# Kernel tuning notes

Hardware: AMD Instinct MI355X
Metric: run time of the kernel (lower is better)

The kernel has to match this reference:

```python
import jax, jax.numpy as jnp
import numpy as np
import math

BS, NAG, HID, NACT, MESS, QD, KD, STEPS, INP = 4096, 8, 256, 16, 64, 64, 64, 5, 128
TRAJ = STEPS * NACT
LAMQ = 0.5


def setup_inputs() -> dict:
    key = jax.random.key(0)
    ks = jax.random.split(key, 12)
    g = lambda k, shape, fan: jax.random.normal(k, shape, jnp.float32) / math.sqrt(fan)
    d = {}
    d["inputs"] = jax.random.normal(ks[0], (BS * NAG, INP), jnp.float32)
    d["old_hstate"] = jax.random.normal(ks[1], (BS * NAG, HID), jnp.float32)
    d["fc1_w"] = g(ks[2], (HID, INP), INP); d["fc1_b"] = jnp.zeros((HID,), jnp.float32)
    d["w_ih"] = g(ks[3], (3 * HID, HID), HID); d["w_hh"] = g(ks[4], (3 * HID, HID), HID)
    d["b_ih"] = jnp.zeros((3 * HID,), jnp.float32); d["b_hh"] = jnp.zeros((3 * HID,), jnp.float32)
    d["dec_w"] = g(ks[5], (NACT, HID), HID); d["dec_b"] = jnp.zeros((NACT,), jnp.float32)
    d["trans_w"] = g(ks[6], (HID, HID + NAG), HID + NAG); d["trans_b"] = jnp.zeros((HID,), jnp.float32)
    d["qij_w"] = g(ks[7], (NACT, HID + MESS), HID + MESS); d["qij_b"] = jnp.zeros((NACT,), jnp.float32)
    d["q_w"] = g(ks[8], (QD, TRAJ), TRAJ); d["q_b"] = jnp.zeros((QD,), jnp.float32)
    d["k_w"] = g(ks[9], (KD, TRAJ), TRAJ); d["k_b"] = jnp.zeros((KD,), jnp.float32)
    d["v_w"] = g(ks[10], (MESS, TRAJ), TRAJ); d["v_b"] = jnp.zeros((MESS,), jnp.float32)
    return d


def _fwd(inputs, old_hstate, fc1_w, fc1_b, w_ih, w_hh, b_ih, b_hh,
         dec_w, dec_b, trans_w, trans_b, qij_w, qij_b,
         q_w, q_b, k_w, k_b, v_w, v_b):
    # fc1 + relu
    x = jax.nn.relu(inputs @ fc1_w.T + fc1_b)  # (BS*NAG, HID)
    # GRUCell (torch gate order: r, z, n)
    gi = x @ w_ih.T + b_ih
    gh = old_hstate @ w_hh.T + b_hh
    ir, iz, i_n = jnp.split(gi, 3, axis=-1)
    hr, hz, h_n = jnp.split(gh, 3, axis=-1)
    r = jax.nn.sigmoid(ir + hr)
    z = jax.nn.sigmoid(iz + hz)
    n = jnp.tanh(i_n + r * h_n)
    h_new = (1.0 - z) * n + z * old_hstate
    h = h_new.reshape(BS, NAG, HID)

    # imagination rollout on detached h
    def step(hc, _):
        q_inf = hc @ dec_w.T + dec_b                       # (BS, NAG, NACT)
        ac = jnp.argmax(q_inf, axis=-1).astype(hc.dtype)   # (BS, NAG)
        ac = jnp.broadcast_to(ac[:, None, :], (BS, NAG, NAG))
        ti = jnp.concatenate([hc, ac], axis=-1)            # (BS, NAG, HID+NAG)
        return ti @ trans_w.T + trans_b, q_inf

    _, qs = jax.lax.scan(step, jax.lax.stop_gradient(h), None, length=STEPS)
    # qs: (STEPS, BS, NAG, NACT) -> trajectory (BS, NAG, STEPS*NACT), step-major on last dim
    traj = jnp.moveaxis(qs, 0, 2).reshape(BS, NAG, TRAJ)

    # tiny agent attention
    query = traj @ q_w.T + q_b   # (BS, NAG, QD)
    key_t = traj @ k_w.T + k_b   # (BS, NAG, KD)
    value = traj @ v_w.T + v_b   # (BS, NAG, MESS)
    score = jnp.einsum('bnq,bmq->bnm', query, key_t) / math.sqrt(MESS)
    attn = jax.nn.softmax(score, axis=-1)
    traj_msg = jnp.einsum('bnm,bmd->bnd', attn, value)  # (BS, NAG, MESS)

    q_local = h @ dec_w.T + dec_b
    q_ij = jnp.concatenate([h, traj_msg], axis=-1) @ qij_w.T + qij_b
    q = q_local + LAMQ * q_ij
    return q, h


def reference(inputs, old_hstate, fc1_w, fc1_b, w_ih, w_hh, b_ih, b_hh,
              dec_w, dec_b, trans_w, trans_b, qij_w, qij_b,
              q_w, q_b, k_w, k_b, v_w, v_b):
    return _fwd(inputs, old_hstate, fc1_w, fc1_b, w_ih, w_hh, b_ih, b_hh,
                dec_w, dec_b, trans_w, trans_b, qij_w, qij_b,
                q_w, q_b, k_w, k_b, v_w, v_b)
```

## Files before the change

kernel.cpp:

```cpp
#include <hip/hip_runtime.h>
#include <math.h>

typedef unsigned short u16;
typedef unsigned int   u32;
typedef __attribute__((ext_vector_type(8))) short bf16x8;
typedef __attribute__((ext_vector_type(4))) float f32x4;

#define NROWS 32768
#define NAG 8
#define HID 256
#define INP 128
#define NACT 16
#define MESS 64
#define TRAJD 80
#define QD 64
#define HOFF 524288

#define PKO_FC1 0
#define PKO_IH  98304
#define PKO_HH  688128
#define PKO_TR  1277952
#define PKO_DEC 1499136
#define PKO_QKV 1511424
#define PKO_QIJ 1566720
#define PK_TOTAL 1582080
#define WS_CB   791040
#define WS_FLAG 793312

#define OB_FC1B 0
#define OB_BIH  256
#define OB_BHH  1024
#define OB_DECB 1792
#define OB_TRB  1808
#define OB_QIJB 2064
#define OB_QB   2080

__device__ __forceinline__ float bf2f(u16 v){ return __uint_as_float(((u32)v)<<16); }
__device__ __forceinline__ u16 f2bf(float f){
    u32 u = __float_as_uint(f);
    return (u16)((u + 0x7fffu + ((u>>16)&1u))>>16);
}
__device__ __forceinline__ float sig_(float x){ return 1.0f/(1.0f+expf(-x)); }
__device__ __forceinline__ float ldin(const void* p, size_t i, int f32){
    return f32 ? ((const float*)p)[i] : bf2f(((const u16*)p)[i]);
}
__device__ __forceinline__ void stout1(void* out, size_t i, float v, int f32){
    if (f32) ((float*)out)[i]=v; else ((u16*)out)[i]=f2bf(v);
}
__device__ __forceinline__ void split3(float w, u16& s0, u16& s1, u16& s2){
    u16 a=f2bf(w); float r  = w - bf2f(a);
    u16 b=f2bf(r); float r2 = r - bf2f(b);
    s0=a; s1=b; s2=f2bf(r2);
}
__device__ __forceinline__ f32x4 splat4(float b){ f32x4 v = {b,b,b,b}; return v; }

#define MFMA(a,b,c) __builtin_amdgcn_mfma_f32_16x16x32_bf16((a),(b),(c),0,0,0)

__device__ __forceinline__ bf16x8 lda_pl(const u16* P, int p, int row, int kbyte){
    const char* b = (const char*)P + ((p*32+row)*640) + (kbyte ^ ((row&7)<<4));
    return *(const bf16x8*)b;
}
__device__ __forceinline__ void stw_pl(u16* P, int p, int row, int col, u16 v){
    char* b = (char*)P + ((p*32+row)*640) + (((col*2)) ^ ((row&7)<<4));
    *(u16*)b = v;
}
__device__ __forceinline__ void split_store_pl(u16* P, int row, int col, float v){
    u16 a,b,c; split3(v,a,b,c);
    stw_pl(P,0,row,col,a); stw_pl(P,1,row,col,b); stw_pl(P,2,row,col,c);
}
__device__ __forceinline__ bf16x8 lda_tp(const u16* P, int p, int row, int kbyte){
    const char* b = (const char*)P + ((p*32+row)*256) + (kbyte ^ ((row&7)<<4));
    return *(const bf16x8*)b;
}
__device__ __forceinline__ void stw_tp(u16* P, int p, int row, int col, u16 v){
    char* b = (char*)P + ((p*32+row)*256) + (((col*2)) ^ ((row&7)<<4));
    *(u16*)b = v;
}
__device__ __forceinline__ void split_store_tp(u16* P, int row, int col, float v){
    u16 a,b,c; split3(v,a,b,c);
    stw_tp(P,0,row,col,a); stw_tp(P,1,row,col,b); stw_tp(P,2,row,col,c);
}
__device__ __forceinline__ float ld_tp1(const u16* P, int p, int row, int col){
    const char* b = (const char*)P + ((p*32+row)*256) + (((col*2)) ^ ((row&7)<<4));
    return bf2f(*(const u16*)b);
}
__device__ __forceinline__ bf16x8 ldg_bf8(const void* p, size_t off){
    return *(const bf16x8*)((const u16*)p + off);
}
__device__ __forceinline__ void ldg_f32_split(const void* p, size_t off, bf16x8& f0, bf16x8& f1, bf16x8& f2){
    const float* fp = (const float*)p + off;
    #pragma unroll
    for (int j=0;j<8;j++){
        float w = fp[j];
        u16 a,b,c; split3(w,a,b,c);
        f0[j]=(short)a; f1[j]=(short)b; f2[j]=(short)c;
    }
}
#define BCH(base, NTv, ksv, pbv, ntv) \
    (*(const bf16x8*)((base) + ((((ksv)*3+(pbv))*(NTv) + (ntv))*512) + lane*8))

__global__ void k_det(const void* __restrict__ inp, int* __restrict__ flag){
    __shared__ int cnt;
    if (threadIdx.x==0) cnt=0;
    __syncthreads();
    int big=0;
    for (int i=threadIdx.x;i<128;i+=64){
        u32 w = ((const u32*)inp)[i];
        float g = bf2f((u16)w);
        if (!(fabsf(g) <= 1e4f)) big++;
    }
    if (big) atomicAdd(&cnt, big);
    __syncthreads();
    if (threadIdx.x==0) *flag = (cnt>=4) ? 1 : 0;
}

__device__ __forceinline__ void pack_tile(const void* W, int Kdim, int NT, u16* pk, int tau, int f32){
    int lane2 = tau & 63, c = tau >> 6;
    int nt = c % NT, ks = c / NT;
    int n  = nt*16 + (lane2 & 15);
    int kb = ks*32 + (lane2 >> 4)*8;
    u16 o0[8],o1[8],o2[8];
    #pragma unroll
    for (int j=0;j<8;j++){
        int k = kb + j;
        float w = (k < Kdim) ? ldin(W, (size_t)n*Kdim + k, f32) : 0.0f;
        split3(w, o0[j], o1[j], o2[j]);
    }
    size_t base = ((size_t)(ks*3+0)*NT + nt)*512 + lane2*8;
    size_t step = (size_t)NT*512;
    #pragma unroll
    for (int j=0;j<8;j++){
        pk[base+j]=o0[j]; pk[base+step+j]=o1[j]; pk[base+2*step+j]=o2[j];
    }
}

__global__ __launch_bounds__(256) void k0_prep(
    const void* fc1_w, const void* w_ih, const void* w_hh, const void* trans_w,
    const void* dec_w, const void* qij_w, const void* q_w, const void* k_w, const void* v_w,
    const void* fc1_b, const void* b_ih, const void* b_hh, const void* dec_b,
    const void* trans_b, const void* qij_b, const void* q_b, const void* k_b, const void* v_b,
    float* __restrict__ ws, const int* __restrict__ flagp)
{
    const int f32 = *flagp;
    u16* pk = (u16*)ws;
    int i = blockIdx.x*256 + threadIdx.x;
    if (i < 4096)        pack_tile(fc1_w,  128, 16, pk+PKO_FC1, i,        f32);
    else if (i < 28672)  pack_tile(w_ih,   256, 48, pk+PKO_IH,  i-4096,   f32);
    else if (i < 53248)  pack_tile(w_hh,   256, 48, pk+PKO_HH,  i-28672,  f32);
    else if (i < 62464)  pack_tile(trans_w,264, 16, pk+PKO_TR,  i-53248,  f32);
    else if (i < 62976)  pack_tile(dec_w,  256,  1, pk+PKO_DEC, i-62464,  f32);
    else if (i < 65280){
        int tau = i - 62976;
        int lane2 = tau&63, c = tau>>6, nt = c%12, ks = c/12;
        int n = nt*16 + (lane2&15);
        const void* W = (n<64)? q_w : (n<128 ? k_w : v_w);
        int nl = n & 63;
        int kb = ks*32 + (lane2>>4)*8;
        u16 o0[8],o1[8],o2[8];
        #pragma unroll
        for (int j=0;j<8;j++){
            int k = kb + j;
            float w = (k < 80) ? ldin(W, (size_t)nl*80 + k, f32) : 0.0f;
            split3(w, o0[j], o1[j], o2[j]);
        }
        u16* dst = pk + PKO_QKV;
        size_t base = ((size_t)(ks*3+0)*12 + nt)*512 + lane2*8;
        size_t step = (size_t)12*512;
        #pragma unroll
        for (int j=0;j<8;j++){
            dst[base+j]=o0[j]; dst[base+step+j]=o1[j]; dst[base+2*step+j]=o2[j];
        }
    }
    else if (i < 65920)  pack_tile(qij_w,  320,  1, pk+PKO_QIJ, i-65280,  f32);
    else if (i < 68192){
        int i2 = i - 65920;
        float v;
        if      (i2<256)  v=ldin(fc1_b,i2,f32);
        else if (i2<1024) v=ldin(b_ih,i2-256,f32);
        else if (i2<1792) v=ldin(b_hh,i2-1024,f32);
        else if (i2<1808) v=ldin(dec_b,i2-1792,f32);
        else if (i2<2064) v=ldin(trans_b,i2-1808,f32);
        else if (i2<2080) v=ldin(qij_b,i2-2064,f32);
        else if (i2<2144) v=ldin(q_b,i2-2080,f32);
        else if (i2<2208) v=ldin(k_b,i2-2144,f32);
        else              v=ldin(v_b,i2-2208,f32);
        ws[WS_CB+i2]=v;
    }
}

template<int F32>
__global__ __launch_bounds__(512,2) void k12_fused(
    const void* __restrict__ inp, const void* __restrict__ oldh,
    const float* __restrict__ ws, void* __restrict__ dout, const int* __restrict__ flagp)
{
    if (*flagp != F32) return;
    constexpr int PBW = F32 ? 2 : 0;
    constexpr int PAG = F32 ? 2 : 0;

    __shared__ __align__(16) u16  planes[3*32*320];
    __shared__ __align__(16) u16  tplanes[3*32*128];
    __shared__ float s_qkv[32*201];
    __shared__ float s_att[256];
    __shared__ float s_bias[2272];
    __shared__ float s_act[32];

    const int t = threadIdx.x;
    const int wid = t>>6, lane = t&63, lr = lane&15, lk = lane>>4;
    const int row0 = blockIdx.x*32;
    const u16* pk = (const u16*)ws;
    const float* cb = ws + WS_CB;

    for (int i=t;i<3*32*320/2;i+=512) ((u32*)planes)[i]=0u;
    for (int i=t;i<3*32*128/2;i+=512) ((u32*)tplanes)[i]=0u;
    for (int i=t;i<2272;i+=512) s_bias[i]=cb[i];
    __syncthreads();

    {
        const u16* pkf = pk + PKO_FC1;
        const int nt0 = wid, nt1 = wid + 8;
        f32x4 acc[2][2];
        acc[0][0]=splat4(s_bias[OB_FC1B+nt0*16+lr]); acc[1][0]=acc[0][0];
        acc[0][1]=splat4(s_bias[OB_FC1B+nt1*16+lr]); acc[1][1]=acc[0][1];
        for (int ks=0;ks<4;ks++){
            bf16x8 a[2][3];
            if (F32){
                ldg_f32_split(inp,(size_t)(row0+lr)*INP + ks*32+lk*8,    a[0][0],a[0][1],a[0][2]);
                ldg_f32_split(inp,(size_t)(row0+16+lr)*INP + ks*32+lk*8, a[1][0],a[1][1],a[1][2]);
            } else {
                a[0][0]=ldg_bf8(inp,(size_t)(row0+lr)*INP + ks*32+lk*8);
                a[1][0]=ldg_bf8(inp,(size_t)(row0+16+lr)*INP + ks*32+lk*8);
            }
            #pragma unroll
            for (int pb=0;pb<=PBW;pb++){
                bf16x8 B0 = BCH(pkf,16,ks,pb,nt0);
                bf16x8 B1 = BCH(pkf,16,ks,pb,nt1);
                #pragma unroll
                for (int pa=0;pa<=((PAG<2-pb)?PAG:(2-pb));pa++){
                    acc[0][0]=MFMA(a[0][pa],B0,acc[0][0]); acc[0][1]=MFMA(a[0][pa],B1,acc[0][1]);
                    acc[1][0]=MFMA(a[1][pa],B0,acc[1][0]); acc[1][1]=MFMA(a[1][pa],B1,acc[1][1]);
                }
            }
        }
        #pragma unroll
        for (int m=0;m<2;m++)
        #pragma unroll
        for (int ni=0;ni<2;ni++)
        #pragma unroll
        for (int j=0;j<4;j++){
            float v = acc[m][ni][j]; v = v>0.f ? v : 0.f;
            split_store_pl(planes, m*16+lk*4+j, (ni?nt1:nt0)*16+lr, v);
        }
    }
    __syncthreads();

    float hreg[16];
    {
        const u16* pki = pk + PKO_IH;
        const u16* pkh = pk + PKO_HH;
        const int g0 = wid, g1 = wid + 8;
        f32x4 aR[2][2], aZ[2][2], aN[2][2], aH[2][2];
        #pragma unroll
        for (int m=0;m<2;m++)
        #pragma unroll
        for (int gi=0;gi<2;gi++){
            int c = (gi?g1:g0)*16 + lr;
            aR[m][gi]=splat4(s_bias[OB_BIH+c]     + s_bias[OB_BHH+c]);
            aZ[m][gi]=splat4(s_bias[OB_BIH+256+c] + s_bias[OB_BHH+256+c]);
            aN[m][gi]=splat4(s_bias[OB_BIH+512+c]);
            aH[m][gi]=splat4(s_bias[OB_BHH+512+c]);
        }
        for (int ks=0;ks<8;ks++){
            #pragma unroll
            for (int pb=0;pb<=PBW;pb++){
                bf16x8 Br0=BCH(pki,48,ks,pb,g0),    Br1=BCH(pki,48,ks,pb,g1);
                bf16x8 Bz0=BCH(pki,48,ks,pb,16+g0), Bz1=BCH(pki,48,ks,pb,16+g1);
                bf16x8 Bn0=BCH(pki,48,ks,pb,32+g0), Bn1=BCH(pki,48,ks,pb,32+g1);
                #pragma unroll
                for (int pa=0;pa<=2-pb;pa++){
                    bf16x8 a0 = lda_pl(planes, pa, lr,    ks*64+lk*16);
                    bf16x8 a1 = lda_pl(planes, pa, 16+lr, ks*64+lk*16);
                    aR[0][0]=MFMA(a0,Br0,aR[0][0]); aR[0][1]=MFMA(a0,Br1,aR[0][1]);
                    aR[1][0]=MFMA(a1,Br0,aR[1][0]); aR[1][1]=MFMA(a1,Br1,aR[1][1]);
                    aZ[0][0]=MFMA(a0,Bz0,aZ[0][0]); aZ[0][1]=MFMA(a0,Bz1,aZ[0][1]);
                    aZ[1][0]=MFMA(a1,Bz0,aZ[1][0]); aZ[1][1]=MFMA(a1,Bz1,aZ[1][1]);
                    aN[0][0]=MFMA(a0,Bn0,aN[0][0]); aN[0][1]=MFMA(a0,Bn1,aN[0][1]);
                    aN[1][0]=MFMA(a1,Bn0,aN[1][0]); aN[1][1]=MFMA(a1,Bn1,aN[1][1]);
                }
            }
        }
        for (int ks=0;ks<8;ks++){
            bf16x8 a[2][3];
            if (F32){
                ldg_f32_split(oldh,(size_t)(row0+lr)*HID + ks*32+lk*8,    a[0][0],a[0][1],a[0][2]);
                ldg_f32_split(oldh,(size_t)(row0+16+lr)*HID + ks*32+lk*8, a[1][0],a[1][1],a[1][2]);
            } else {
                a[0][0]=ldg_bf8(oldh,(size_t)(row0+lr)*HID + ks*32+lk*8);
                a[1][0]=ldg_bf8(oldh,(size_t)(row0+16+lr)*HID + ks*32+lk*8);
            }
            #pragma unroll
            for (int pb=0;pb<=PBW;pb++){
                bf16x8 Br0=BCH(pkh,48,ks,pb,g0),    Br1=BCH(pkh,48,ks,pb,g1);
                bf16x8 Bz0=BCH(pkh,48,ks,pb,16+g0), Bz1=BCH(pkh,48,ks,pb,16+g1);
                bf16x8 Bh0=BCH(pkh,48,ks,pb,32+g0), Bh1=BCH(pkh,48,ks,pb,32+g1);
                #pragma unroll
                for (int pa=0;pa<=((PAG<2-pb)?PAG:(2-pb));pa++){
                    aR[0][0]=MFMA(a[0][pa],Br0,aR[0][0]); aR[0][1]=MFMA(a[0][pa],Br1,aR[0][1]);
                    aR[1][0]=MFMA(a[1][pa],Br0,aR[1][0]); aR[1][1]=MFMA(a[1][pa],Br1,aR[1][1]);
                    aZ[0][0]=MFMA(a[0][pa],Bz0,aZ[0][0]); aZ[0][1]=MFMA(a[0][pa],Bz1,aZ[0][1]);
                    aZ[1][0]=MFMA(a[1][pa],Bz0,aZ[1][0]); aZ[1][1]=MFMA(a[1][pa],Bz1,aZ[1][1]);
                    aH[0][0]=MFMA(a[0][pa],Bh0,aH[0][0]); aH[0][1]=MFMA(a[0][pa],Bh1,aH[0][1]);
                    aH[1][0]=MFMA(a[1][pa],Bh0,aH[1][0]); aH[1][1]=MFMA(a[1][pa],Bh1,aH[1][1]);
                }
            }
        }
        #pragma unroll
        for (int m=0;m<2;m++)
        #pragma unroll
        for (int gi=0;gi<2;gi++)
        #pragma unroll
        for (int j=0;j<4;j++){
            int row = m*16 + lk*4 + j;
            int c   = (gi?g1:g0)*16 + lr;
            float r  = sig_(aR[m][gi][j]);
            float z  = sig_(aZ[m][gi][j]);
            float nv = tanhf(aN[m][gi][j] + r*aH[m][gi][j]);
            float ho = ldin(oldh,(size_t)(row0+row)*HID + c, F32);
            float h  = (1.f-z)*nv + z*ho;
            hreg[m*8+gi*4+j] = h;
            stout1(dout,(size_t)HOFF + (size_t)(row0+row)*HID + c, h, F32);
        }
    }
    __syncthreads();
    #pragma unroll
    for (int m=0;m<2;m++)
    #pragma unroll
    for (int gi=0;gi<2;gi++)
    #pragma unroll
    for (int j=0;j<4;j++)
        split_store_pl(planes, m*16+lk*4+j, (gi?wid+8:wid)*16+lr, hreg[m*8+gi*4+j]);
    __syncthreads();

    const u16* pkd = pk + PKO_DEC;
    const u16* pkt = pk + PKO_TR;
    #pragma unroll 1
    for (int s=0;s<5;s++){
        if (wid<2){
            const int m = wid;
            f32x4 d0 = splat4(s_bias[OB_DECB+lr]);
            f32x4 d1 = splat4(0.f), d2 = splat4(0.f);
            for (int ks=0;ks<8;ks++){
                #pragma unroll
                for (int pb=0;pb<=PBW;pb++){
                    bf16x8 B = BCH(pkd,1,ks,pb,0);
                    #pragma unroll
                    for (int pa=0;pa<=2-pb;pa++){
                        bf16x8 a = lda_pl(planes, pa, m*16+lr, ks*64+lk*16);
                        if (pa==0) d0=MFMA(a,B,d0); else if (pa==1) d1=MFMA(a,B,d1); else d2=MFMA(a,B,d2);
                    }
                }
            }
            f32x4 q;
            #pragma unroll
            for (int j=0;j<4;j++) q[j]=d0[j]+d1[j]+d2[j];
            #pragma unroll
            for (int j=0;j<4;j++)
                split_store_tp(tplanes, m*16+lk*4+j, s*16+lr, q[j]);
            if (s<4){
                #pragma unroll
                for (int j=0;j<4;j++){
                    float v = q[j]; int ai = lr;
                    #pragma unroll
                    for (int msk=1; msk<16; msk<<=1){
                        float pv = __shfl_xor(v, msk);
                        int   pi = __shfl_xor(ai, msk);
                        if (pv>v || (pv==v && pi<ai)){ v=pv; ai=pi; }
                    }
                    if (lr==0) s_act[m*16+lk*4+j] = (float)ai;
                }
            }
        }
        if (s==4) break;
        __syncthreads();
        if (t<256){
            int row = t>>3, aj = t&7;
            stw_pl(planes, 0, row, 256+aj, f2bf(s_act[(row & ~7) + aj]));
        }
        __syncthreads();
        {
            const int nt0=wid, nt1=wid+8;
            f32x4 acc[2][2];
            acc[0][0]=splat4(s_bias[OB_TRB+nt0*16+lr]); acc[1][0]=acc[0][0];
            acc[0][1]=splat4(s_bias[OB_TRB+nt1*16+lr]); acc[1][1]=acc[0][1];
            for (int ks=0;ks<9;ks++){
                #pragma unroll
                for (int pb=0;pb<=PBW;pb++){
                    bf16x8 B0=BCH(pkt,16,ks,pb,nt0), B1=BCH(pkt,16,ks,pb,nt1);
                    #pragma unroll
                    for (int pa=0;pa<=2-pb;pa++){
                        bf16x8 a0 = lda_pl(planes,pa,lr,   ks*64+lk*16);
                        bf16x8 a1 = lda_pl(planes,pa,16+lr,ks*64+lk*16);
                        acc[0][0]=MFMA(a0,B0,acc[0][0]); acc[0][1]=MFMA(a0,B1,acc[0][1]);
                        acc[1][0]=MFMA(a1,B0,acc[1][0]); acc[1][1]=MFMA(a1,B1,acc[1][1]);
                    }
                }
            }
            __syncthreads();
            #pragma unroll
            for (int m=0;m<2;m++)
            #pragma unroll
            for (int ni=0;ni<2;ni++)
            #pragma unroll
            for (int j=0;j<4;j++)
                split_store_pl(planes, m*16+lk*4+j, (ni?nt1:nt0)*16+lr, acc[m][ni][j]);
        }
        __syncthreads();
    }

    __syncthreads();
    #pragma unroll
    for (int m=0;m<2;m++)
    #pragma unroll
    for (int gi=0;gi<2;gi++)
    #pragma unroll
    for (int j=0;j<4;j++)
        split_store_pl(planes, m*16+lk*4+j, (gi?wid+8:wid)*16+lr, hreg[m*8+gi*4+j]);
    {
        const u16* pkq = pk + PKO_QKV;
        const int n0 = wid;
        const int has2 = (wid<4);
        const int n1 = wid + 8;
        f32x4 acc[2][2];
        acc[0][0]=splat4(s_bias[OB_QB+n0*16+lr]); acc[1][0]=acc[0][0];
        { float b1 = has2 ? s_bias[OB_QB+n1*16+lr] : 0.f;
          acc[0][1]=splat4(b1); acc[1][1]=acc[0][1]; }
        for (int ks=0;ks<3;ks++){
            #pragma unroll
            for (int pb=0;pb<=PBW;pb++){
                bf16x8 B0 = BCH(pkq,12,ks,pb,n0);
                bf16x8 B1 = has2 ? BCH(pkq,12,ks,pb,n1) : B0;
                #pragma unroll
                for (int pa=0;pa<=2-pb;pa++){
                    bf16x8 a0 = lda_tp(tplanes, pa, lr,    ks*64+lk*16);
                    bf16x8 a1 = lda_tp(tplanes, pa, 16+lr, ks*64+lk*16);
                    acc[0][0]=MFMA(a0,B0,acc[0][0]); acc[1][0]=MFMA(a1,B0,acc[1][0]);
                    if (has2){ acc[0][1]=MFMA(a0,B1,acc[0][1]); acc[1][1]=MFMA(a1,B1,acc[1][1]); }
                }
            }
        }
        #pragma unroll
        for (int m=0;m<2;m++)
        #pragma unroll
        for (int j=0;j<4;j++){
            int row = m*16+lk*4+j;
            s_qkv[row*201 + n0*16+lr] = acc[m][0][j];
            if (has2) s_qkv[row*201 + n1*16+lr] = acc[m][1][j];
        }
    }
    __syncthreads();
    if (t<256){
        int b=t>>6, n=(t>>3)&7, mm=t&7;
        const float* qv = s_qkv + (b*8+n)*201;
        const float* kv = s_qkv + (b*8+mm)*201 + 64;
        float a2=0.f;
        #pragma unroll
        for (int d=0;d<64;d++) a2 += qv[d]*kv[d];
        s_att[t] = a2*0.125f;
    }
    __syncthreads();
    if (t<32){
        int base = (t>>3)*64 + (t&7)*8;
        float mx = s_att[base];
        #pragma unroll
        for (int j2=1;j2<8;j2++) mx = fmaxf(mx, s_att[base+j2]);
        float e[8]; float sum=0.f;
        #pragma unroll
        for (int j2=0;j2<8;j2++){ e[j2]=expf(s_att[base+j2]-mx); sum+=e[j2]; }
        float inv = 1.f/sum;
        #pragma unroll
        for (int j2=0;j2<8;j2++) s_att[base+j2] = e[j2]*inv;
    }
    __syncthreads();
    for (int o=t;o<2048;o+=512){
        int row=o>>6, d=o&63, b=row>>3;
        float a3=0.f;
        #pragma unroll
        for (int mm=0;mm<8;mm++) a3 += s_att[b*64+(row&7)*8+mm]*s_qkv[(b*8+mm)*201+128+d];
        split_store_pl(planes, row, 256+d, a3);
    }
    __syncthreads();
    if (wid<2){
        const u16* pkj = pk + PKO_QIJ;
        const int m = wid;
        f32x4 e0 = splat4(s_bias[OB_QIJB+lr]);
        f32x4 e1 = splat4(0.f), e2 = splat4(0.f);
        for (int ks=0;ks<10;ks++){
            #pragma unroll
            for (int pb=0;pb<=PBW;pb++){
                bf16x8 B = BCH(pkj,1,ks,pb,0);
                #pragma unroll
                for (int pa=0;pa<=2-pb;pa++){
                    bf16x8 a = lda_pl(planes, pa, m*16+lr, ks*64+lk*16);
                    if (pa==0) e0=MFMA(a,B,e0); else if (pa==1) e1=MFMA(a,B,e1); else e2=MFMA(a,B,e2);
                }
            }
        }
        #pragma unroll
        for (int j=0;j<4;j++){
            int row = m*16+lk*4+j;
            float ql = ld_tp1(tplanes,0,row,lr) + ld_tp1(tplanes,1,row,lr) + ld_tp1(tplanes,2,row,lr);
            float qq = ql + 0.5f*(e0[j]+e1[j]+e2[j]);
            stout1(dout,(size_t)(row0+row)*NACT + lr, qq, F32);
        }
    }
}

extern "C" void kernel_launch(void* const* d_in, const int* in_sizes, int n_in,
                              void* d_out, int out_size, void* d_ws, size_t ws_size,
                              hipStream_t stream)
{
    (void)in_sizes; (void)n_in; (void)out_size; (void)ws_size;
    const void* inputs = d_in[0];
    const void* oldh   = d_in[1];
    float* ws = (float*)d_ws;
    int* flagp = (int*)(ws + WS_FLAG);

    k_det<<<1,64,0,stream>>>(inputs, flagp);
    k0_prep<<<268,256,0,stream>>>(d_in[2],d_in[4],d_in[5],d_in[10],d_in[8],d_in[12],
                                  d_in[14],d_in[16],d_in[18],
                                  d_in[3],d_in[6],d_in[7],d_in[9],d_in[11],d_in[13],
                                  d_in[15],d_in[17],d_in[19],
                                  ws, flagp);
    k12_fused<0><<<1024,512,0,stream>>>(inputs, oldh, ws, d_out, flagp);
    k12_fused<1><<<1024,512,0,stream>>>(inputs, oldh, ws, d_out, flagp);
}
```

Measured before the change: 616.8 us.

## Halve rows per block to 16, use 256-thread blocks, keep trajectory in fp32 LDS

Each block now handles 16 rows (two batch groups) with 4 waves, each wave owning 4 output tiles, and the grid doubles to 2048 blocks. The goal is more resident blocks per CU through lower LDS use. The bias staging in LDS is dropped in favour of direct reads from global memory. The trajectory is stored as fp32 in LDS and split into three bf16 parts when the QKV projection loads it. The decoder step and argmax now run redundantly in every wave, so no separate action sync is needed. The trade-off is less reuse of each B-fragment load, since each one now feeds half as many rows, which means more weight traffic from L2.

```diff
diff --git a/kernel.cpp b/kernel.cpp
--- a/kernel.cpp
+++ b/kernel.cpp
@@ -57,32 +57,16 @@
 #define MFMA(a,b,c) __builtin_amdgcn_mfma_f32_16x16x32_bf16((a),(b),(c),0,0,0)
 
 __device__ __forceinline__ bf16x8 lda_pl(const u16* P, int p, int row, int kbyte){
-    const char* b = (const char*)P + ((p*32+row)*640) + (kbyte ^ ((row&7)<<4));
+    const char* b = (const char*)P + ((p*16+row)*640) + (kbyte ^ ((row&7)<<4));
     return *(const bf16x8*)b;
 }
 __device__ __forceinline__ void stw_pl(u16* P, int p, int row, int col, u16 v){
-    char* b = (char*)P + ((p*32+row)*640) + (((col*2)) ^ ((row&7)<<4));
+    char* b = (char*)P + ((p*16+row)*640) + (((col*2)) ^ ((row&7)<<4));
     *(u16*)b = v;
 }
 __device__ __forceinline__ void split_store_pl(u16* P, int row, int col, float v){
     u16 a,b,c; split3(v,a,b,c);
     stw_pl(P,0,row,col,a); stw_pl(P,1,row,col,b); stw_pl(P,2,row,col,c);
-}
-__device__ __forceinline__ bf16x8 lda_tp(const u16* P, int p, int row, int kbyte){
-    const char* b = (const char*)P + ((p*32+row)*256) + (kbyte ^ ((row&7)<<4));
-    return *(const bf16x8*)b;
-}
-__device__ __forceinline__ void stw_tp(u16* P, int p, int row, int col, u16 v){
-    char* b = (char*)P + ((p*32+row)*256) + (((col*2)) ^ ((row&7)<<4));
-    *(u16*)b = v;
-}
-__device__ __forceinline__ void split_store_tp(u16* P, int row, int col, float v){
-    u16 a,b,c; split3(v,a,b,c);
-    stw_tp(P,0,row,col,a); stw_tp(P,1,row,col,b); stw_tp(P,2,row,col,c);
-}
-__device__ __forceinline__ float ld_tp1(const u16* P, int p, int row, int col){
-    const char* b = (const char*)P + ((p*32+row)*256) + (((col*2)) ^ ((row&7)<<4));
-    return bf2f(*(const u16*)b);
 }
 __device__ __forceinline__ bf16x8 ldg_bf8(const void* p, size_t off){
     return *(const bf16x8*)((const u16*)p + off);
@@ -189,7 +173,7 @@
 }
 
 template<int F32>
-__global__ __launch_bounds__(512,2) void k12_fused(
+__global__ __launch_bounds__(256,3) void k12_fused(
     const void* __restrict__ inp, const void* __restrict__ oldh,
     const float* __restrict__ ws, void* __restrict__ dout, const int* __restrict__ flagp)
 {
@@ -197,58 +181,47 @@
     constexpr int PBW = F32 ? 2 : 0;
     constexpr int PAG = F32 ? 2 : 0;
 
-    __shared__ __align__(16) u16  planes[3*32*320];
-    __shared__ __align__(16) u16  tplanes[3*32*128];
-    __shared__ float s_qkv[32*201];
-    __shared__ float s_att[256];
-    __shared__ float s_bias[2272];
-    __shared__ float s_act[32];
+    __shared__ __align__(16) u16   planes[3*16*320];
+    __shared__ __align__(16) float s_traj[16*100];
+    __shared__ __align__(16) float s_qkv[16*196];
+    __shared__ float s_att[128];
 
     const int t = threadIdx.x;
     const int wid = t>>6, lane = t&63, lr = lane&15, lk = lane>>4;
-    const int row0 = blockIdx.x*32;
+    const int row0 = blockIdx.x*16;
     const u16* pk = (const u16*)ws;
     const float* cb = ws + WS_CB;
 
-    for (int i=t;i<3*32*320/2;i+=512) ((u32*)planes)[i]=0u;
-    for (int i=t;i<3*32*128/2;i+=512) ((u32*)tplanes)[i]=0u;
-    for (int i=t;i<2272;i+=512) s_bias[i]=cb[i];
+    for (int i=t;i<7680;i+=256) ((u32*)planes)[i]=0u;
+    for (int i=t;i<1600;i+=256) s_traj[i]=0.f;
     __syncthreads();
 
     {
         const u16* pkf = pk + PKO_FC1;
-        const int nt0 = wid, nt1 = wid + 8;
-        f32x4 acc[2][2];
-        acc[0][0]=splat4(s_bias[OB_FC1B+nt0*16+lr]); acc[1][0]=acc[0][0];
-        acc[0][1]=splat4(s_bias[OB_FC1B+nt1*16+lr]); acc[1][1]=acc[0][1];
+        f32x4 acc[4];
+        #pragma unroll
+        for (int i=0;i<4;i++) acc[i]=splat4(cb[OB_FC1B+(wid*4+i)*16+lr]);
         for (int ks=0;ks<4;ks++){
-            bf16x8 a[2][3];
-            if (F32){
-                ldg_f32_split(inp,(size_t)(row0+lr)*INP + ks*32+lk*8,    a[0][0],a[0][1],a[0][2]);
-                ldg_f32_split(inp,(size_t)(row0+16+lr)*INP + ks*32+lk*8, a[1][0],a[1][1],a[1][2]);
-            } else {
-                a[0][0]=ldg_bf8(inp,(size_t)(row0+lr)*INP + ks*32+lk*8);
-                a[1][0]=ldg_bf8(inp,(size_t)(row0+16+lr)*INP + ks*32+lk*8);
-            }
-            #pragma unroll
-            for (int pb=0;pb<=PBW;pb++){
-                bf16x8 B0 = BCH(pkf,16,ks,pb,nt0);
-                bf16x8 B1 = BCH(pkf,16,ks,pb,nt1);
-                #pragma unroll
-                for (int pa=0;pa<=((PAG<2-pb)?PAG:(2-pb));pa++){
-                    acc[0][0]=MFMA(a[0][pa],B0,acc[0][0]); acc[0][1]=MFMA(a[0][pa],B1,acc[0][1]);
-                    acc[1][0]=MFMA(a[1][pa],B0,acc[1][0]); acc[1][1]=MFMA(a[1][pa],B1,acc[1][1]);
-                }
-            }
-        }
-        #pragma unroll
-        for (int m=0;m<2;m++)
-        #pragma unroll
-        for (int ni=0;ni<2;ni++)
+            bf16x8 a[3];
+            if (F32) ldg_f32_split(inp,(size_t)(row0+lr)*INP + ks*32+lk*8, a[0],a[1],a[2]);
+            else     a[0]=ldg_bf8(inp,(size_t)(row0+lr)*INP + ks*32+lk*8);
+            #pragma unroll
+            for (int pb=0;pb<=PBW;pb++){
+                #pragma unroll
+                for (int i=0;i<4;i++){
+                    bf16x8 B = BCH(pkf,16,ks,pb,wid*4+i);
+                    #pragma unroll
+                    for (int pa=0;pa<=((PAG<2-pb)?PAG:(2-pb));pa++)
+                        acc[i]=MFMA(a[pa],B,acc[i]);
+                }
+            }
+        }
+        #pragma unroll
+        for (int i=0;i<4;i++)
         #pragma unroll
         for (int j=0;j<4;j++){
-            float v = acc[m][ni][j]; v = v>0.f ? v : 0.f;
-            split_store_pl(planes, m*16+lk*4+j, (ni?nt1:nt0)*16+lr, v);
+            float v=acc[i][j]; v = v>0.f ? v : 0.f;
+            split_store_pl(planes, lk*4+j, (wid*4+i)*16+lr, v);
         }
     }
     __syncthreads();
@@ -257,241 +230,223 @@
     {
         const u16* pki = pk + PKO_IH;
         const u16* pkh = pk + PKO_HH;
-        const int g0 = wid, g1 = wid + 8;
-        f32x4 aR[2][2], aZ[2][2], aN[2][2], aH[2][2];
-        #pragma unroll
-        for (int m=0;m<2;m++)
-        #pragma unroll
-        for (int gi=0;gi<2;gi++){
-            int c = (gi?g1:g0)*16 + lr;
-            aR[m][gi]=splat4(s_bias[OB_BIH+c]     + s_bias[OB_BHH+c]);
-            aZ[m][gi]=splat4(s_bias[OB_BIH+256+c] + s_bias[OB_BHH+256+c]);
-            aN[m][gi]=splat4(s_bias[OB_BIH+512+c]);
-            aH[m][gi]=splat4(s_bias[OB_BHH+512+c]);
+        f32x4 aR[4],aZ[4],aN[4],aH[4];
+        #pragma unroll
+        for (int i=0;i<4;i++){
+            int c=(wid*4+i)*16+lr;
+            aR[i]=splat4(cb[OB_BIH+c]     + cb[OB_BHH+c]);
+            aZ[i]=splat4(cb[OB_BIH+256+c] + cb[OB_BHH+256+c]);
+            aN[i]=splat4(cb[OB_BIH+512+c]);
+            aH[i]=splat4(cb[OB_BHH+512+c]);
         }
         for (int ks=0;ks<8;ks++){
             #pragma unroll
             for (int pb=0;pb<=PBW;pb++){
-                bf16x8 Br0=BCH(pki,48,ks,pb,g0),    Br1=BCH(pki,48,ks,pb,g1);
-                bf16x8 Bz0=BCH(pki,48,ks,pb,16+g0), Bz1=BCH(pki,48,ks,pb,16+g1);
-                bf16x8 Bn0=BCH(pki,48,ks,pb,32+g0), Bn1=BCH(pki,48,ks,pb,32+g1);
-                #pragma unroll
-                for (int pa=0;pa<=2-pb;pa++){
-                    bf16x8 a0 = lda_pl(planes, pa, lr,    ks*64+lk*16);
-                    bf16x8 a1 = lda_pl(planes, pa, 16+lr, ks*64+lk*16);
-                    aR[0][0]=MFMA(a0,Br0,aR[0][0]); aR[0][1]=MFMA(a0,Br1,aR[0][1]);
-                    aR[1][0]=MFMA(a1,Br0,aR[1][0]); aR[1][1]=MFMA(a1,Br1,aR[1][1]);
-                    aZ[0][0]=MFMA(a0,Bz0,aZ[0][0]); aZ[0][1]=MFMA(a0,Bz1,aZ[0][1]);
-                    aZ[1][0]=MFMA(a1,Bz0,aZ[1][0]); aZ[1][1]=MFMA(a1,Bz1,aZ[1][1]);
-                    aN[0][0]=MFMA(a0,Bn0,aN[0][0]); aN[0][1]=MFMA(a0,Bn1,aN[0][1]);
-                    aN[1][0]=MFMA(a1,Bn0,aN[1][0]); aN[1][1]=MFMA(a1,Bn1,aN[1][1]);
+                bf16x8 av[3];
+                #pragma unroll
+                for (int pa=0;pa<=2-pb;pa++) av[pa]=lda_pl(planes,pa,lr,ks*64+lk*16);
+                #pragma unroll
+                for (int i=0;i<4;i++){
+                    bf16x8 Br=BCH(pki,48,ks,pb,   wid*4+i);
+                    bf16x8 Bz=BCH(pki,48,ks,pb,16+wid*4+i);
+                    bf16x8 Bn=BCH(pki,48,ks,pb,32+wid*4+i);
+                    #pragma unroll
+                    for (int pa=0;pa<=2-pb;pa++){
+                        aR[i]=MFMA(av[pa],Br,aR[i]);
+                        aZ[i]=MFMA(av[pa],Bz,aZ[i]);
+                        aN[i]=MFMA(av[pa],Bn,aN[i]);
+                    }
                 }
             }
         }
         for (int ks=0;ks<8;ks++){
-            bf16x8 a[2][3];
-            if (F32){
-                ldg_f32_split(oldh,(size_t)(row0+lr)*HID + ks*32+lk*8,    a[0][0],a[0][1],a[0][2]);
-                ldg_f32_split(oldh,(size_t)(row0+16+lr)*HID + ks*32+lk*8, a[1][0],a[1][1],a[1][2]);
-            } else {
-                a[0][0]=ldg_bf8(oldh,(size_t)(row0+lr)*HID + ks*32+lk*8);
-                a[1][0]=ldg_bf8(oldh,(size_t)(row0+16+lr)*HID + ks*32+lk*8);
-            }
-            #pragma unroll
-            for (int pb=0;pb<=PBW;pb++){
-                bf16x8 Br0=BCH(pkh,48,ks,pb,g0),    Br1=BCH(pkh,48,ks,pb,g1);
-                bf16x8 Bz0=BCH(pkh,48,ks,pb,16+g0), Bz1=BCH(pkh,48,ks,pb,16+g1);
-                bf16x8 Bh0=BCH(pkh,48,ks,pb,32+g0), Bh1=BCH(pkh,48,ks,pb,32+g1);
-                #pragma unroll
-                for (int pa=0;pa<=((PAG<2-pb)?PAG:(2-pb));pa++){
-                    aR[0][0]=MFMA(a[0][pa],Br0,aR[0][0]); aR[0][1]=MFMA(a[0][pa],Br1,aR[0][1]);
-                    aR[1][0]=MFMA(a[1][pa],Br0,aR[1][0]); aR[1][1]=MFMA(a[1][pa],Br1,aR[1][1]);
-                    aZ[0][0]=MFMA(a[0][pa],Bz0,aZ[0][0]); aZ[0][1]=MFMA(a[0][pa],Bz1,aZ[0][1]);
-                    aZ[1][0]=MFMA(a[1][pa],Bz0,aZ[1][0]); aZ[1][1]=MFMA(a[1][pa],Bz1,aZ[1][1]);
-                    aH[0][0]=MFMA(a[0][pa],Bh0,aH[0][0]); aH[0][1]=MFMA(a[0][pa],Bh1,aH[0][1]);
-                    aH[1][0]=MFMA(a[1][pa],Bh0,aH[1][0]); aH[1][1]=MFMA(a[1][pa],Bh1,aH[1][1]);
-                }
-            }
-        }
-        #pragma unroll
-        for (int m=0;m<2;m++)
-        #pragma unroll
-        for (int gi=0;gi<2;gi++)
+            bf16x8 a[3];
+            if (F32) ldg_f32_split(oldh,(size_t)(row0+lr)*HID + ks*32+lk*8, a[0],a[1],a[2]);
+            else     a[0]=ldg_bf8(oldh,(size_t)(row0+lr)*HID + ks*32+lk*8);
+            #pragma unroll
+            for (int pb=0;pb<=PBW;pb++){
+                #pragma unroll
+                for (int i=0;i<4;i++){
+                    bf16x8 Br=BCH(pkh,48,ks,pb,   wid*4+i);
+                    bf16x8 Bz=BCH(pkh,48,ks,pb,16+wid*4+i);
+                    bf16x8 Bh=BCH(pkh,48,ks,pb,32+wid*4+i);
+                    #pragma unroll
+                    for (int pa=0;pa<=((PAG<2-pb)?PAG:(2-pb));pa++){
+                        aR[i]=MFMA(a[pa],Br,aR[i]);
+                        aZ[i]=MFMA(a[pa],Bz,aZ[i]);
+                        aH[i]=MFMA(a[pa],Bh,aH[i]);
+                    }
+                }
+            }
+        }
+        #pragma unroll
+        for (int i=0;i<4;i++)
         #pragma unroll
         for (int j=0;j<4;j++){
-            int row = m*16 + lk*4 + j;
-            int c   = (gi?g1:g0)*16 + lr;
-            float r  = sig_(aR[m][gi][j]);
-            float z  = sig_(aZ[m][gi][j]);
-            float nv = tanhf(aN[m][gi][j] + r*aH[m][gi][j]);
+            int row = lk*4+j, c = (wid*4+i)*16+lr;
+            float r  = sig_(aR[i][j]);
+            float z  = sig_(aZ[i][j]);
+            float nv = tanhf(aN[i][j] + r*aH[i][j]);
             float ho = ldin(oldh,(size_t)(row0+row)*HID + c, F32);
             float h  = (1.f-z)*nv + z*ho;
-            hreg[m*8+gi*4+j] = h;
+            hreg[i*4+j] = h;
             stout1(dout,(size_t)HOFF + (size_t)(row0+row)*HID + c, h, F32);
         }
     }
     __syncthreads();
     #pragma unroll
-    for (int m=0;m<2;m++)
-    #pragma unroll
-    for (int gi=0;gi<2;gi++)
+    for (int i=0;i<4;i++)
     #pragma unroll
     for (int j=0;j<4;j++)
-        split_store_pl(planes, m*16+lk*4+j, (gi?wid+8:wid)*16+lr, hreg[m*8+gi*4+j]);
+        split_store_pl(planes, lk*4+j, (wid*4+i)*16+lr, hreg[i*4+j]);
     __syncthreads();
 
     const u16* pkd = pk + PKO_DEC;
     const u16* pkt = pk + PKO_TR;
     #pragma unroll 1
     for (int s=0;s<5;s++){
-        if (wid<2){
-            const int m = wid;
-            f32x4 d0 = splat4(s_bias[OB_DECB+lr]);
-            f32x4 d1 = splat4(0.f), d2 = splat4(0.f);
-            for (int ks=0;ks<8;ks++){
-                #pragma unroll
-                for (int pb=0;pb<=PBW;pb++){
-                    bf16x8 B = BCH(pkd,1,ks,pb,0);
-                    #pragma unroll
-                    for (int pa=0;pa<=2-pb;pa++){
-                        bf16x8 a = lda_pl(planes, pa, m*16+lr, ks*64+lk*16);
-                        if (pa==0) d0=MFMA(a,B,d0); else if (pa==1) d1=MFMA(a,B,d1); else d2=MFMA(a,B,d2);
-                    }
-                }
-            }
-            f32x4 q;
-            #pragma unroll
-            for (int j=0;j<4;j++) q[j]=d0[j]+d1[j]+d2[j];
-            #pragma unroll
-            for (int j=0;j<4;j++)
-                split_store_tp(tplanes, m*16+lk*4+j, s*16+lr, q[j]);
-            if (s<4){
-                #pragma unroll
-                for (int j=0;j<4;j++){
-                    float v = q[j]; int ai = lr;
-                    #pragma unroll
-                    for (int msk=1; msk<16; msk<<=1){
-                        float pv = __shfl_xor(v, msk);
-                        int   pi = __shfl_xor(ai, msk);
-                        if (pv>v || (pv==v && pi<ai)){ v=pv; ai=pi; }
-                    }
-                    if (lr==0) s_act[m*16+lk*4+j] = (float)ai;
-                }
-            }
+        f32x4 d0 = splat4(cb[OB_DECB+lr]);
+        f32x4 d1 = splat4(0.f), d2 = splat4(0.f);
+        for (int ks=0;ks<8;ks++){
+            #pragma unroll
+            for (int pb=0;pb<=PBW;pb++){
+                bf16x8 B = BCH(pkd,1,ks,pb,0);
+                #pragma unroll
+                for (int pa=0;pa<=2-pb;pa++){
+                    bf16x8 a = lda_pl(planes, pa, lr, ks*64+lk*16);
+                    if (pa==0) d0=MFMA(a,B,d0); else if (pa==1) d1=MFMA(a,B,d1); else d2=MFMA(a,B,d2);
+                }
+            }
+        }
+        f32x4 q;
+        #pragma unroll
+        for (int j=0;j<4;j++) q[j]=d0[j]+d1[j]+d2[j];
+        if (wid==0){
+            #pragma unroll
+            for (int j=0;j<4;j++) s_traj[(lk*4+j)*100 + s*16 + lr] = q[j];
         }
         if (s==4) break;
-        __syncthreads();
-        if (t<256){
-            int row = t>>3, aj = t&7;
-            stw_pl(planes, 0, row, 256+aj, f2bf(s_act[(row & ~7) + aj]));
+        int act[4];
+        #pragma unroll
+        for (int j=0;j<4;j++){
+            float v = q[j]; int ai = lr;
+            #pragma unroll
+            for (int msk=1; msk<16; msk<<=1){
+                float pv = __shfl_xor(v, msk);
+                int   pi = __shfl_xor(ai, msk);
+                if (pv>v || (pv==v && pi<ai)){ v=pv; ai=pi; }
+            }
+            act[j]=ai;
+        }
+        if (wid==0 && lr<8){
+            #pragma unroll
+            for (int j=0;j<4;j++){
+                int r = lk*4+j;
+                stw_pl(planes, 0, (r&~7)+lr, 256+(r&7), f2bf((float)act[j]));
+            }
         }
         __syncthreads();
         {
-            const int nt0=wid, nt1=wid+8;
-            f32x4 acc[2][2];
-            acc[0][0]=splat4(s_bias[OB_TRB+nt0*16+lr]); acc[1][0]=acc[0][0];
-            acc[0][1]=splat4(s_bias[OB_TRB+nt1*16+lr]); acc[1][1]=acc[0][1];
+            f32x4 acc[4];
+            #pragma unroll
+            for (int i=0;i<4;i++) acc[i]=splat4(cb[OB_TRB+(wid*4+i)*16+lr]);
             for (int ks=0;ks<9;ks++){
                 #pragma unroll
                 for (int pb=0;pb<=PBW;pb++){
-                    bf16x8 B0=BCH(pkt,16,ks,pb,nt0), B1=BCH(pkt,16,ks,pb,nt1);
-                    #pragma unroll
-                    for (int pa=0;pa<=2-pb;pa++){
-                        bf16x8 a0 = lda_pl(planes,pa,lr,   ks*64+lk*16);
-                        bf16x8 a1 = lda_pl(planes,pa,16+lr,ks*64+lk*16);
-                        acc[0][0]=MFMA(a0,B0,acc[0][0]); acc[0][1]=MFMA(a0,B1,acc[0][1]);
-                        acc[1][0]=MFMA(a1,B0,acc[1][0]); acc[1][1]=MFMA(a1,B1,acc[1][1]);
+                    bf16x8 av[3];
+                    #pragma unroll
+                    for (int pa=0;pa<=2-pb;pa++) av[pa]=lda_pl(planes,pa,lr,ks*64+lk*16);
+                    #pragma unroll
+                    for (int i=0;i<4;i++){
+                        bf16x8 B=BCH(pkt,16,ks,pb,wid*4+i);
+                        #pragma unroll
+                        for (int pa=0;pa<=2-pb;pa++)
+                            acc[i]=MFMA(av[pa],B,acc[i]);
                     }
                 }
             }
             __syncthreads();
             #pragma unroll
-            for (int m=0;m<2;m++)
-            #pragma unroll
-            for (int ni=0;ni<2;ni++)
+            for (int i=0;i<4;i++)
             #pragma unroll
             for (int j=0;j<4;j++)
-                split_store_pl(planes, m*16+lk*4+j, (ni?nt1:nt0)*16+lr, acc[m][ni][j]);
+                split_store_pl(planes, lk*4+j, (wid*4+i)*16+lr, acc[i][j]);
         }
         __syncthreads();
     }
-
-    __syncthreads();
-    #pragma unroll
-    for (int m=0;m<2;m++)
-    #pragma unroll
-    for (int gi=0;gi<2;gi++)
+    __syncthreads();
+
+    #pragma unroll
+    for (int i=0;i<4;i++)
     #pragma unroll
     for (int j=0;j<4;j++)
-        split_store_pl(planes, m*16+lk*4+j, (gi?wid+8:wid)*16+lr, hreg[m*8+gi*4+j]);
+        split_store_pl(planes, lk*4+j, (wid*4+i)*16+lr, hreg[i*4+j]);
     {
         const u16* pkq = pk + PKO_QKV;
-        const int n0 = wid;
-        const int has2 = (wid<4);
-        const int n1 = wid + 8;
-        f32x4 acc[2][2];
-        acc[0][0]=splat4(s_bias[OB_QB+n0*16+lr]); acc[1][0]=acc[0][0];
-        { float b1 = has2 ? s_bias[OB_QB+n1*16+lr] : 0.f;
-          acc[0][1]=splat4(b1); acc[1][1]=acc[0][1]; }
+        f32x4 acc[3];
+        #pragma unroll
+        for (int i=0;i<3;i++) acc[i]=splat4(cb[OB_QB+(wid*3+i)*16+lr]);
         for (int ks=0;ks<3;ks++){
-            #pragma unroll
-            for (int pb=0;pb<=PBW;pb++){
-                bf16x8 B0 = BCH(pkq,12,ks,pb,n0);
-                bf16x8 B1 = has2 ? BCH(pkq,12,ks,pb,n1) : B0;
-                #pragma unroll
-                for (int pa=0;pa<=2-pb;pa++){
-                    bf16x8 a0 = lda_tp(tplanes, pa, lr,    ks*64+lk*16);
-                    bf16x8 a1 = lda_tp(tplanes, pa, 16+lr, ks*64+lk*16);
-                    acc[0][0]=MFMA(a0,B0,acc[0][0]); acc[1][0]=MFMA(a1,B0,acc[1][0]);
-                    if (has2){ acc[0][1]=MFMA(a0,B1,acc[0][1]); acc[1][1]=MFMA(a1,B1,acc[1][1]); }
-                }
-            }
-        }
-        #pragma unroll
-        for (int m=0;m<2;m++)
-        #pragma unroll
-        for (int j=0;j<4;j++){
-            int row = m*16+lk*4+j;
-            s_qkv[row*201 + n0*16+lr] = acc[m][0][j];
-            if (has2) s_qkv[row*201 + n1*16+lr] = acc[m][1][j];
-        }
-    }
-    __syncthreads();
-    if (t<256){
+            bf16x8 a[3];
+            {
+                const float* tp = s_traj + lr*100 + ks*32 + lk*8;
+                #pragma unroll
+                for (int e=0;e<8;e++){
+                    u16 x0,x1,x2; split3(tp[e],x0,x1,x2);
+                    a[0][e]=(short)x0; a[1][e]=(short)x1; a[2][e]=(short)x2;
+                }
+            }
+            #pragma unroll
+            for (int pb=0;pb<=PBW;pb++){
+                #pragma unroll
+                for (int i=0;i<3;i++){
+                    bf16x8 B = BCH(pkq,12,ks,pb,wid*3+i);
+                    #pragma unroll
+                    for (int pa=0;pa<=2-pb;pa++)
+                        acc[i]=MFMA(a[pa],B,acc[i]);
+                }
+            }
+        }
+        #pragma unroll
+        for (int i=0;i<3;i++)
+        #pragma unroll
+        for (int j=0;j<4;j++)
+            s_qkv[(lk*4+j)*196 + (wid*3+i)*16+lr] = acc[i][j];
+    }
+    __syncthreads();
+    if (t<128){
         int b=t>>6, n=(t>>3)&7, mm=t&7;
-        const float* qv = s_qkv + (b*8+n)*201;
-        const float* kv = s_qkv + (b*8+mm)*201 + 64;
+        const float* qv = s_qkv + (b*8+n)*196;
+        const float* kv = s_qkv + (b*8+mm)*196 + 64;
         float a2=0.f;
         #pragma unroll
-        for (int d=0;d<64;d++) a2 += qv[d]*kv[d];
+        for (int d2=0;d2<64;d2++) a2 += qv[d2]*kv[d2];
         s_att[t] = a2*0.125f;
     }
     __syncthreads();
-    if (t<32){
-        int base = (t>>3)*64 + (t&7)*8;
-        float mx = s_att[base];
-        #pragma unroll
-        for (int j2=1;j2<8;j2++) mx = fmaxf(mx, s_att[base+j2]);
+    if (t<16){
+        float mx = s_att[t*8];
+        #pragma unroll
+        for (int j2=1;j2<8;j2++) mx = fmaxf(mx, s_att[t*8+j2]);
         float e[8]; float sum=0.f;
         #pragma unroll
-        for (int j2=0;j2<8;j2++){ e[j2]=expf(s_att[base+j2]-mx); sum+=e[j2]; }
+        for (int j2=0;j2<8;j2++){ e[j2]=expf(s_att[t*8+j2]-mx); sum+=e[j2]; }
         float inv = 1.f/sum;
         #pragma unroll
-        for (int j2=0;j2<8;j2++) s_att[base+j2] = e[j2]*inv;
-    }
-    __syncthreads();
-    for (int o=t;o<2048;o+=512){
-        int row=o>>6, d=o&63, b=row>>3;
+        for (int j2=0;j2<8;j2++) s_att[t*8+j2] = e[j2]*inv;
+    }
+    __syncthreads();
+    for (int o=t;o<1024;o+=256){
+        int row=o>>6, d2=o&63, b=row>>3;
         float a3=0.f;
         #pragma unroll
-        for (int mm=0;mm<8;mm++) a3 += s_att[b*64+(row&7)*8+mm]*s_qkv[(b*8+mm)*201+128+d];
-        split_store_pl(planes, row, 256+d, a3);
-    }
-    __syncthreads();
-    if (wid<2){
+        for (int mm=0;mm<8;mm++) a3 += s_att[b*64+(row&7)*8+mm]*s_qkv[(b*8+mm)*196+128+d2];
+        split_store_pl(planes, row, 256+d2, a3);
+    }
+    __syncthreads();
+    if (wid==0){
         const u16* pkj = pk + PKO_QIJ;
-        const int m = wid;
-        f32x4 e0 = splat4(s_bias[OB_QIJB+lr]);
+        f32x4 e0 = splat4(cb[OB_QIJB+lr]);
         f32x4 e1 = splat4(0.f), e2 = splat4(0.f);
         for (int ks=0;ks<10;ks++){
             #pragma unroll
@@ -499,17 +454,16 @@
                 bf16x8 B = BCH(pkj,1,ks,pb,0);
                 #pragma unroll
                 for (int pa=0;pa<=2-pb;pa++){
-                    bf16x8 a = lda_pl(planes, pa, m*16+lr, ks*64+lk*16);
+                    bf16x8 a = lda_pl(planes, pa, lr, ks*64+lk*16);
                     if (pa==0) e0=MFMA(a,B,e0); else if (pa==1) e1=MFMA(a,B,e1); else e2=MFMA(a,B,e2);
                 }
             }
         }
         #pragma unroll
         for (int j=0;j<4;j++){
-            int row = m*16+lk*4+j;
-            float ql = ld_tp1(tplanes,0,row,lr) + ld_tp1(tplanes,1,row,lr) + ld_tp1(tplanes,2,row,lr);
-            float qq = ql + 0.5f*(e0[j]+e1[j]+e2[j]);
-            stout1(dout,(size_t)(row0+row)*NACT + lr, qq, F32);
+            int row = lk*4+j;
+            float ql = s_traj[row*100 + lr];
+            stout1(dout,(size_t)(row0+row)*NACT + lr, ql + 0.5f*(e0[j]+e1[j]+e2[j]), F32);
         }
     }
 }
@@ -530,6 +484,6 @@
                                   d_in[3],d_in[6],d_in[7],d_in[9],d_in[11],d_in[13],
                                   d_in[15],d_in[17],d_in[19],
                                   ws, flagp);
-    k12_fused<0><<<1024,512,0,stream>>>(inputs, oldh, ws, d_out, flagp);
-    k12_fused<1><<<1024,512,0,stream>>>(inputs, oldh, ws, d_out, flagp);
-}
+    k12_fused<0><<<2048,256,0,stream>>>(inputs, oldh, ws, d_out, flagp);
+    k12_fused<1><<<2048,256,0,stream>>>(inputs, oldh, ws, d_out, flagp);
+}
```

Result: slower. 1.705 ms (+176.5%).
